# Performance work log

Hardware: AMD Instinct MI355X
Metric: run time of the kernel (lower is better)

Reference implementation:

```python
import jax, jax.numpy as jnp
import numpy as np

END_CLAUSE, PRED, ARG_FUNC, ARG_VAR = 0, 1, 2, 3
NUM_ACTION_TYPES = 8
NUM_LAYERS = 3


def _ln(x, g, b, eps=1e-5):
    m = jnp.mean(x, -1, keepdims=True)
    v = jnp.var(x, -1, keepdims=True)
    return (x - m) * jax.lax.rsqrt(v + eps) * g + b


def _ssm_block(x, Win, b_in, Wdt, b_dt, Alog, WB, b_B, WC, b_C, Dp, Wout, b_out, g, b):
    # x: [B,T,D]
    res = x
    xz = x @ Win.T + b_in
    x_ssm, z = jnp.split(xz, 2, axis=-1)
    z = jax.nn.silu(z)
    dt = jax.nn.softplus(x_ssm @ Wdt.T + b_dt)   # [B,T,D]
    Bm = x_ssm @ WB.T + b_B                       # [B,T,N]
    Cm = x_ssm @ WC.T + b_C                       # [B,T,N]
    A = -jnp.exp(Alog)                            # [D,N]

    def step(h, inp):
        x_t, dt_t, B_t, C_t = inp                 # [B,D],[B,D],[B,N],[B,N]
        dA = jnp.exp(A[None] * dt_t[:, :, None])  # [B,D,N]
        h = dA * h + (dt_t * x_t)[:, :, None] * B_t[:, None, :]
        return h, jnp.einsum('bdn,bn->bd', h, C_t)

    h0 = jnp.zeros((x.shape[0], Alog.shape[0], Alog.shape[1]), x.dtype)
    xs = tuple(jnp.swapaxes(a, 0, 1) for a in (x_ssm, dt, Bm, Cm))
    _, ys = jax.lax.scan(step, h0, xs)
    y = jnp.swapaxes(ys, 0, 1)                    # [B,T,D]
    y = (y + Dp * x_ssm) * z
    y = y @ Wout.T + b_out
    return _ln(y + res, g, b)


def _forward(symbol_embeds, memory, action_embed, W_arg, b_arg, var_embed, W_comb, b_comb,
             Win, b_in, Wdt, b_dt, Alog, WB, b_B, WC, b_C, Dp, Wout, b_out, ssm_g, ssm_b,
             Wm, b_m, Wg, b_g, cn_g, cn_b, Wa, b_a, Wq, b_q, Wk, b_k, Wv, b_v,
             target_actions, target_arguments, symbol_mask):
    B, T = target_actions.shape
    S = symbol_embeds.shape[1]
    D = symbol_embeds.shape[2]
    MV = var_embed.shape[0]
    # teacher-forcing shift with END_CLAUSE BOS
    dec_a = jnp.concatenate([jnp.full((B, 1), END_CLAUSE, target_actions.dtype), target_actions[:, :-1]], 1)
    dec_g = jnp.concatenate([jnp.zeros((B, 1), target_arguments.dtype), target_arguments[:, :-1]], 1)
    act_emb = action_embed[dec_a]                                          # [B,T,D]
    sym = symbol_embeds[jnp.arange(B)[:, None], jnp.clip(dec_g, 0, S - 1)]  # [B,T,D]
    ptr_emb = sym @ W_arg.T + b_arg
    var_emb_t = var_embed[jnp.clip(dec_g, 0, MV - 1)]
    ptr_mask = (dec_a == PRED) | (dec_a == ARG_FUNC)
    vmask = dec_a == ARG_VAR
    arg_emb = jnp.where(ptr_mask[..., None], ptr_emb,
                        jnp.where(vmask[..., None], var_emb_t, jnp.zeros((), symbol_embeds.dtype)))
    h = jnp.concatenate([act_emb, arg_emb], -1) @ W_comb.T + b_comb
    mem_summary = memory.mean(1)  # zero padding included, matching torch code
    for l in range(NUM_LAYERS):
        h = _ssm_block(h, Win[l], b_in[l], Wdt[l], b_dt[l], Alog[l], WB[l], b_B[l], WC[l], b_C[l],
                       Dp[l], Wout[l], b_out[l], ssm_g[l], ssm_b[l])
        ctx = jnp.broadcast_to((mem_summary @ Wm[l].T + b_m[l])[:, None, :], h.shape)
        gate = jax.nn.sigmoid(jnp.concatenate([h, ctx], -1) @ Wg[l].T + b_g[l])
        h = _ln(h + gate * ctx, cn_g[l], cn_b[l])
    action_logits = h @ Wa.T + b_a
    scores = jnp.einsum('btd,bsd->bts', h @ Wq.T + b_q, symbol_embeds @ Wk.T + b_k) / (float(D) ** 0.5)
    scores = jnp.where(symbol_mask[:, None, :], scores, -jnp.inf)
    var_logits = h @ Wv.T + b_v
    return action_logits, scores, var_logits


def setup_inputs() -> dict:
    B, T, S, M, D, N, L, NA, MV = 8, 1024, 128, 512, 512, 16, NUM_LAYERS, NUM_ACTION_TYPES, 20
    keys = iter(jax.random.split(jax.random.key(0), 48))

    def nrm(shape, scale=1.0):
        return jax.random.normal(next(keys), shape, jnp.float32) * scale

    s = 1.0 / np.sqrt(D)
    s2 = 1.0 / np.sqrt(2 * D)
    inp = dict(
        symbol_embeds=nrm((B, S, D)), memory=nrm((B, M, D)),
        action_embed=nrm((NA, D), 0.02), W_arg=nrm((D, D), s), b_arg=jnp.zeros((D,)),
        var_embed=nrm((MV, D), 0.02), W_comb=nrm((D, 2 * D), s2), b_comb=jnp.zeros((D,)),
        Win=nrm((L, 2 * D, D), s), b_in=jnp.zeros((L, 2 * D)),
        Wdt=nrm((L, D, D), s), b_dt=jnp.zeros((L, D)),
        Alog=nrm((L, D, N)),
        WB=nrm((L, N, D), s), b_B=jnp.zeros((L, N)),
        WC=nrm((L, N, D), s), b_C=jnp.zeros((L, N)),
        Dp=jnp.ones((L, D)),
        Wout=nrm((L, D, D), s), b_out=jnp.zeros((L, D)),
        ssm_g=jnp.ones((L, D)), ssm_b=jnp.zeros((L, D)),
        Wm=nrm((L, D, D), s), b_m=jnp.zeros((L, D)),
        Wg=nrm((L, D, 2 * D), s2), b_g=jnp.zeros((L, D)),
        cn_g=jnp.ones((L, D)), cn_b=jnp.zeros((L, D)),
        Wa=nrm((NA, D), s), b_a=jnp.zeros((NA,)),
        Wq=nrm((D, D), s), b_q=jnp.zeros((D,)),
        Wk=nrm((D, D), s), b_k=jnp.zeros((D,)),
        Wv=nrm((MV, D), s), b_v=jnp.zeros((MV,)),
        target_actions=jax.random.randint(next(keys), (B, T), 0, NA),
        target_arguments=jax.random.randint(next(keys), (B, T), 0, S),
    )
    counts = jax.random.randint(next(keys), (B,), S // 2, S + 1)
    inp['symbol_mask'] = jnp.arange(S)[None, :] < counts[:, None]
    return inp


def reference(symbol_embeds, memory, action_embed, W_arg, b_arg, var_embed, W_comb, b_comb,
              Win, b_in, Wdt, b_dt, Alog, WB, b_B, WC, b_C, Dp, Wout, b_out, ssm_g, ssm_b,
              Wm, b_m, Wg, b_g, cn_g, cn_b, Wa, b_a, Wq, b_q, Wk, b_k, Wv, b_v,
              target_actions, target_arguments, symbol_mask):
    return _forward(symbol_embeds, memory, action_embed, W_arg, b_arg, var_embed, W_comb, b_comb,
                    Win, b_in, Wdt, b_dt, Alog, WB, b_B, WC, b_C, Dp, Wout, b_out, ssm_g, ssm_b,
                    Wm, b_m, Wg, b_g, cn_g, cn_b, Wa, b_a, Wq, b_q, Wk, b_k, Wv, b_v,
                    target_actions, target_arguments, symbol_mask)
```

## Files before the change

### kernel.cpp

```cpp
#include <hip/hip_runtime.h>
#include <math.h>

#define R_  8192
#define T_  1024
#define B_  8
#define S_  128
#define D_  512
#define N_  16
#define MV_ 20
#define NA_ 8
#define MM_ 512

#define TC  4
#define LCH 256
#define TS  32
#define DB  8

typedef __attribute__((ext_vector_type(8))) short short8;
typedef __attribute__((ext_vector_type(4))) float f32x4;

static __device__ __forceinline__ float sigmoidf_(float x) {
  return 1.f / (1.f + __expf(-x));
}

static __device__ __forceinline__ void split2(float x0, float x1,
                                              unsigned& hp, unsigned& lp) {
  unsigned u0 = __float_as_uint(x0), u1 = __float_as_uint(x1);
  unsigned r0 = u0 + 0x7fffu + ((u0 >> 16) & 1u);
  unsigned r1 = u1 + 0x7fffu + ((u1 >> 16) & 1u);
  hp = __builtin_amdgcn_perm(r1, r0, 0x07060302u);
  float l0 = x0 - __uint_as_float(r0 & 0xffff0000u);
  float l1 = x1 - __uint_as_float(r1 & 0xffff0000u);
  lp = __builtin_amdgcn_perm(__float_as_uint(l1), __float_as_uint(l0),
                             0x07060302u);
}

static __device__ __forceinline__ float row16_sum(float v) {
  v += __int_as_float(__builtin_amdgcn_update_dpp(0, __float_as_int(v), 0xB1, 0xF, 0xF, true));
  v += __int_as_float(__builtin_amdgcn_update_dpp(0, __float_as_int(v), 0x4E, 0xF, 0xF, true));
  v += __int_as_float(__builtin_amdgcn_update_dpp(0, __float_as_int(v), 0x141, 0xF, 0xF, true));
  v += __int_as_float(__builtin_amdgcn_update_dpp(0, __float_as_int(v), 0x140, 0xF, 0xF, true));
  return v;
}

#define KP 40

__global__ void __launch_bounds__(256) gemm_bx3(
    const float* __restrict__ A, int lda,
    const unsigned short* __restrict__ Wh, const unsigned short* __restrict__ Wl,
    const float* __restrict__ bias,
    const float* __restrict__ bbias,
    float* __restrict__ C, int ldc,
    int K, int act,
    float* __restrict__ aux1, float* __restrict__ aux2)
{
  __shared__ unsigned short Ah[128 * KP], Al[128 * KP];
  __shared__ unsigned short Bh[64 * KP],  Bl[64 * KP];
  const int tid = threadIdx.x;
  const int m0 = blockIdx.y << 7;
  const int n0 = blockIdx.x << 6;
  const int lane = tid & 63;
  const int wm = ((tid >> 6) & 1) << 6;
  const int wn = (tid >> 7) << 5;
  const int lr = lane & 15, quad = lane >> 4;

  const int arow = tid >> 1, akoff = (tid & 1) << 4;
  const float* ap = A + (size_t)(m0 + arow) * lda + akoff;
  const int brow = tid >> 2, bkoff = (tid & 3) << 3;
  const unsigned short* wph = Wh + (size_t)(n0 + brow) * K + bkoff;
  const unsigned short* wpl = Wl + (size_t)(n0 + brow) * K + bkoff;

  f32x4 acc[4][2];
#pragma unroll
  for (int mt = 0; mt < 4; ++mt)
#pragma unroll
    for (int nt = 0; nt < 2; ++nt)
      acc[mt][nt] = (f32x4){0.f, 0.f, 0.f, 0.f};

  for (int k0 = 0; k0 < K; k0 += 32) {
    float4 av[4];
#pragma unroll
    for (int i = 0; i < 4; ++i) av[i] = *(const float4*)(ap + k0 + (i << 2));
    uint4 bh = *(const uint4*)(wph + k0);
    uint4 bl = *(const uint4*)(wpl + k0);
    __syncthreads();
    {
      float af[16] = {av[0].x, av[0].y, av[0].z, av[0].w,
                      av[1].x, av[1].y, av[1].z, av[1].w,
                      av[2].x, av[2].y, av[2].z, av[2].w,
                      av[3].x, av[3].y, av[3].z, av[3].w};
#pragma unroll
      for (int g = 0; g < 2; ++g) {
        unsigned h4[4], l4[4];
#pragma unroll
        for (int p = 0; p < 4; ++p)
          split2(af[g * 8 + 2 * p], af[g * 8 + 2 * p + 1], h4[p], l4[p]);
        *(uint4*)&Ah[arow * KP + akoff + (g << 3)] = make_uint4(h4[0], h4[1], h4[2], h4[3]);
        *(uint4*)&Al[arow * KP + akoff + (g << 3)] = make_uint4(l4[0], l4[1], l4[2], l4[3]);
      }
    }
    *(uint4*)&Bh[brow * KP + bkoff] = bh;
    *(uint4*)&Bl[brow * KP + bkoff] = bl;
    __syncthreads();

    short8 fah[4], fal[4], fbh[2], fbl[2];
#pragma unroll
    for (int mt = 0; mt < 4; ++mt) {
      int r = (wm + mt * 16 + lr) * KP + quad * 8;
      fah[mt] = *(const short8*)&Ah[r];
      fal[mt] = *(const short8*)&Al[r];
    }
#pragma unroll
    for (int nt = 0; nt < 2; ++nt) {
      int r = (wn + nt * 16 + lr) * KP + quad * 8;
      fbh[nt] = *(const short8*)&Bh[r];
      fbl[nt] = *(const short8*)&Bl[r];
    }
#pragma unroll
    for (int mt = 0; mt < 4; ++mt)
#pragma unroll
      for (int nt = 0; nt < 2; ++nt) {
        acc[mt][nt] = __builtin_amdgcn_mfma_f32_16x16x32_bf16(
            fah[mt], fbl[nt], acc[mt][nt], 0, 0, 0);
        acc[mt][nt] = __builtin_amdgcn_mfma_f32_16x16x32_bf16(
            fal[mt], fbh[nt], acc[mt][nt], 0, 0, 0);
        acc[mt][nt] = __builtin_amdgcn_mfma_f32_16x16x32_bf16(
            fah[mt], fbh[nt], acc[mt][nt], 0, 0, 0);
      }
  }

  const int bb = m0 >> 10;
#pragma unroll
  for (int mt = 0; mt < 4; ++mt)
#pragma unroll
    for (int nt = 0; nt < 2; ++nt) {
      int ncol = n0 + wn + nt * 16 + lr;
      float bv = bias ? bias[ncol] : 0.f;
      if (bbias) bv += bbias[(size_t)bb * ldc + ncol];
#pragma unroll
      for (int reg = 0; reg < 4; ++reg) {
        int m = m0 + wm + mt * 16 + quad * 4 + reg;
        float v = acc[mt][nt][reg] + bv;
        if (act == 0) {
          C[(size_t)m * ldc + ncol] = v;
        } else if (act == 1) {
          C[(size_t)m * ldc + ncol] = (v > 20.f) ? v : log1pf(__expf(v));
        } else if (act == 2) {
          C[(size_t)m * ldc + ncol] = sigmoidf_(v);
        } else if (act == 3) {
          if (ncol < 512)      C[(size_t)m * 512 + ncol] = (v > 20.f) ? v : log1pf(__expf(v));
          else if (ncol < 528) aux1[(size_t)m * 16 + (ncol - 512)] = v;
          else if (ncol < 544) aux2[(size_t)m * 16 + (ncol - 528)] = v;
        } else {
          if (ncol < 512)      C[(size_t)m * 512 + ncol] = v;
          else if (ncol < 520) aux1[(size_t)m * 8 + (ncol - 512)] = v;
          else if (ncol < 540) aux2[(size_t)m * 20 + (ncol - 520)] = v;
        }
      }
    }
}

__global__ void wcvt(const float* __restrict__ W, int ldw,
                     unsigned short* __restrict__ hi, unsigned short* __restrict__ lo)
{
  int gid = blockIdx.x * 256 + threadIdx.x;
  int base = gid << 3;
  int r = base >> 9, c = base & 511;
  const float* p = W + (size_t)r * ldw + c;
  float4 a0 = *(const float4*)p, a1 = *(const float4*)(p + 4);
  float af[8] = {a0.x, a0.y, a0.z, a0.w, a1.x, a1.y, a1.z, a1.w};
  unsigned h4[4], l4[4];
#pragma unroll
  for (int p2 = 0; p2 < 4; ++p2) split2(af[2 * p2], af[2 * p2 + 1], h4[p2], l4[p2]);
  *(uint4*)&hi[(size_t)r * 512 + c] = make_uint4(h4[0], h4[1], h4[2], h4[3]);
  *(uint4*)&lo[(size_t)r * 512 + c] = make_uint4(l4[0], l4[1], l4[2], l4[3]);
}

__global__ void pack_w_bf(unsigned short* __restrict__ hi, unsigned short* __restrict__ lo,
                          float* __restrict__ bd,
                          const float* __restrict__ w0, const float* __restrict__ b0,
                          const float* __restrict__ w1, const float* __restrict__ b1,
                          const float* __restrict__ w2, const float* __restrict__ b2,
                          int n1, int n2)
{
  int gid = blockIdx.x * 256 + threadIdx.x;
  int base = gid << 3;
  int r = base >> 9, c = base & 511;
  const float* src = nullptr;
  if (r < 512)                 src = w0 + (size_t)r * 512 + c;
  else if (r < 512 + n1)       src = w1 + (size_t)(r - 512) * 512 + c;
  else if (r < 512 + n1 + n2)  src = w2 + (size_t)(r - 512 - n1) * 512 + c;
  float af[8] = {0.f};
  if (src) {
    float4 a0 = *(const float4*)src, a1 = *(const float4*)(src + 4);
    af[0]=a0.x; af[1]=a0.y; af[2]=a0.z; af[3]=a0.w;
    af[4]=a1.x; af[5]=a1.y; af[6]=a1.z; af[7]=a1.w;
  }
  unsigned h4[4], l4[4];
#pragma unroll
  for (int p2 = 0; p2 < 4; ++p2) split2(af[2 * p2], af[2 * p2 + 1], h4[p2], l4[p2]);
  *(uint4*)&hi[(size_t)r * 512 + c] = make_uint4(h4[0], h4[1], h4[2], h4[3]);
  *(uint4*)&lo[(size_t)r * 512 + c] = make_uint4(l4[0], l4[1], l4[2], l4[3]);
  if (c == 0) {
    float bvv = 0.f;
    if (r < 512)                 bvv = b0[r];
    else if (r < 512 + n1)       bvv = b1[r - 512];
    else if (r < 512 + n1 + n2)  bvv = b2[r - 512 - n1];
    bd[r] = bvv;
  }
}

#define BM 64
#define BN 64
#define BK 16

__global__ void __launch_bounds__(256) scores_kernel(
    const float* __restrict__ q, const float* __restrict__ kmat,
    const int* __restrict__ mask, float* __restrict__ out)
{
  __shared__ __align__(16) float As[BK][BM + 4];
  __shared__ __align__(16) float Ws[BK][BN + 4];
  const int b = blockIdx.z;
  const float* A = q + (size_t)b * T_ * D_;
  const float* W = kmat + (size_t)b * S_ * D_;
  const int tid = threadIdx.x;
  const int m0 = blockIdx.y * BM;
  const int n0 = blockIdx.x * BN;
  const int tx = tid & 15, ty = tid >> 4;
  const int lr = tid >> 2;
  const int lk = (tid & 3) << 2;
  float acc[4][4] = {{0.f}};
  const float* aptr = A + (size_t)(m0 + lr) * D_ + lk;
  const float* wptr = W + (size_t)(n0 + lr) * D_ + lk;

  for (int k0 = 0; k0 < D_; k0 += BK) {
    float4 av = *(const float4*)(aptr + k0);
    float4 wv = *(const float4*)(wptr + k0);
    __syncthreads();
    As[lk + 0][lr] = av.x; As[lk + 1][lr] = av.y;
    As[lk + 2][lr] = av.z; As[lk + 3][lr] = av.w;
    Ws[lk + 0][lr] = wv.x; Ws[lk + 1][lr] = wv.y;
    Ws[lk + 2][lr] = wv.z; Ws[lk + 3][lr] = wv.w;
    __syncthreads();
#pragma unroll
    for (int kk = 0; kk < BK; ++kk) {
      float4 a4 = *(const float4*)&As[kk][ty << 2];
      float4 b4 = *(const float4*)&Ws[kk][tx << 2];
      float a_[4] = {a4.x, a4.y, a4.z, a4.w};
      float b_[4] = {b4.x, b4.y, b4.z, b4.w};
#pragma unroll
      for (int i = 0; i < 4; ++i)
#pragma unroll
        for (int j = 0; j < 4; ++j)
          acc[i][j] = fmaf(a_[i], b_[j], acc[i][j]);
    }
  }

  const float scale = 0.044194173824159216f;
#pragma unroll
  for (int i = 0; i < 4; ++i) {
    int t = m0 + (ty << 2) + i;
#pragma unroll
    for (int j = 0; j < 4; ++j) {
      int s = n0 + (tx << 2) + j;
      float v = acc[i][j] * scale;
      if (mask[b * S_ + s] == 0) v = -1e30f;
      out[((size_t)(b * T_ + t)) * S_ + s] = v;
    }
  }
}

__global__ void gemm_small(const float* __restrict__ A, int lda,
                           const float* __restrict__ W, int ldw,
                           const float* __restrict__ bias,
                           float* __restrict__ C, int ldc,
                           int MN, int Ncols, int K)
{
  int gid = blockIdx.x * 256 + threadIdx.x;
  if (gid >= MN) return;
  int r = gid / Ncols, o = gid - r * Ncols;
  const float4* a = (const float4*)(A + (size_t)r * lda);
  const float4* w = (const float4*)(W + (size_t)o * ldw);
  float acc = bias ? bias[o] : 0.f;
  int K4 = K >> 2;
  for (int k = 0; k < K4; ++k) {
    float4 av = a[k], wv = w[k];
    acc = fmaf(av.x, wv.x, fmaf(av.y, wv.y, fmaf(av.z, wv.z, fmaf(av.w, wv.w, acc))));
  }
  C[(size_t)r * ldc + o] = acc;
}

__global__ void ctx_kernel(const float* __restrict__ msum, const float* __restrict__ Wm,
                           const float* __restrict__ b_m, float* __restrict__ ctxv)
{
  int gid = blockIdx.x * 256 + threadIdx.x;
  int l = gid >> 12, b = (gid >> 9) & 7, dd = gid & 511;
  const float4* a = (const float4*)(msum + b * 512);
  const float4* w = (const float4*)(Wm + ((size_t)l * 512 + dd) * 512);
  float acc = b_m[l * 512 + dd];
  for (int k = 0; k < 128; ++k) {
    float4 av = a[k], wv = w[k];
    acc = fmaf(av.x, wv.x, fmaf(av.y, wv.y, fmaf(av.z, wv.z, fmaf(av.w, wv.w, acc))));
  }
  ctxv[gid] = acc;
}

__global__ void gctx_kernel(const float* __restrict__ ctxv, const float* __restrict__ Wg,
                            const float* __restrict__ b_g, float* __restrict__ gctx)
{
  int gid = blockIdx.x * 256 + threadIdx.x;
  int l = gid >> 12, b = (gid >> 9) & 7, dd = gid & 511;
  const float4* a = (const float4*)(ctxv + ((size_t)l * 8 + b) * 512);
  const float4* w = (const float4*)(Wg + ((size_t)l * 512 + dd) * 1024 + 512);
  float acc = b_g[l * 512 + dd];
  for (int k = 0; k < 128; ++k) {
    float4 av = a[k], wv = w[k];
    acc = fmaf(av.x, wv.x, fmaf(av.y, wv.y, fmaf(av.z, wv.z, fmaf(av.w, wv.w, acc))));
  }
  gctx[gid] = acc;
}

__global__ void __launch_bounds__(256) transpose512(
    const float* __restrict__ A, float* __restrict__ At)
{
  __shared__ float tl[32][33];
  int i0 = blockIdx.y * 32, j0 = blockIdx.x * 32;
  int li = threadIdx.x & 31, lj = threadIdx.x >> 5;
#pragma unroll
  for (int k = 0; k < 4; ++k)
    tl[lj * 4 + k][li] = A[(size_t)(i0 + lj * 4 + k) * 512 + j0 + li];
  __syncthreads();
#pragma unroll
  for (int k = 0; k < 4; ++k)
    At[(size_t)(j0 + lj * 4 + k) * 512 + i0 + li] = tl[li][lj * 4 + k];
}

__global__ void memsum_kernel(const float* __restrict__ mem, float* __restrict__ out)
{
  int b = blockIdx.x >> 1;
  int d = ((blockIdx.x & 1) << 8) + threadIdx.x;
  const float* p = mem + (size_t)b * MM_ * D_ + d;
  float s = 0.f;
  for (int m = 0; m < MM_; ++m) s += p[(size_t)m * D_];
  out[b * D_ + d] = s * (1.f / MM_);
}

__global__ void combine_kernel(float* __restrict__ h, const float* __restrict__ Psym,
                               const float* __restrict__ Pact,
                               const float* __restrict__ Pvar, const float* __restrict__ b2,
                               const float* __restrict__ bcomb,
                               const int* __restrict__ ta, const int* __restrict__ tg)
{
  int i = blockIdx.x * 256 + threadIdx.x;
  int r = i >> 9, j = i & 511;
  int t = r & (T_ - 1);
  int a = t ? ta[r - 1] : 0;
  float val = Pact[a * D_ + j] + bcomb[j];
  if (a == 1 || a == 2) {
    int g = t ? tg[r - 1] : 0;
    g = g < 0 ? 0 : (g > S_ - 1 ? S_ - 1 : g);
    val += Psym[((size_t)(r >> 10) * S_ + g) * D_ + j] + b2[j];
  } else if (a == 3) {
    int g = t ? tg[r - 1] : 0;
    g = g < 0 ? 0 : (g > MV_ - 1 ? MV_ - 1 : g);
    val += Pvar[g * D_ + j];
  }
  h[i] = val;
}

__global__ void __launch_bounds__(128) scan_pass1(
    const float* __restrict__ xz, const float* __restrict__ dts,
    const float* __restrict__ Bmv, const float* __restrict__ Alog,
    float* __restrict__ aprod, float* __restrict__ hend)
{
  __shared__ __align__(8) float sdt[TS][DB];
  __shared__ __align__(8) float sx[TS][DB];
  __shared__ __align__(16) float sB[TS][16];
  const int tid = threadIdx.x;
  const int n = tid & 15, dl = tid >> 4;
  const int c = blockIdx.x, db = blockIdx.y, b = blockIdx.z;
  const int d = (db << 3) + dl;
  const int t0 = c * LCH;
  const int lrow = tid >> 2;
  const int lc2 = (tid & 3) << 1;
  const int bc4 = (tid & 3) << 2;

  float An = -__expf(Alog[d * N_ + n]);
  float hst = 0.f, dsum = 0.f;

  for (int tt = 0; tt < LCH; tt += TS) {
    __syncthreads();
    {
      size_t gr = (size_t)b * T_ + t0 + tt + lrow;
      *(float2*)&sdt[lrow][lc2] = *(const float2*)&dts[(gr << 9) + (db << 3) + lc2];
      *(float2*)&sx[lrow][lc2]  = *(const float2*)&xz[(gr << 10) + (db << 3) + lc2];
      *(float4*)&sB[lrow][bc4]  = *(const float4*)&Bmv[gr * N_ + bc4];
    }
    __syncthreads();
#pragma unroll 8
    for (int s = 0; s < TS; ++s) {
      float dtv = sdt[s][dl], xv = sx[s][dl], Bv = sB[s][n];
      float dA = __expf(An * dtv);
      hst = fmaf(dA, hst, dtv * xv * Bv);
      dsum += dtv;
    }
  }
  size_t idx = (size_t)c * (B_ * D_ * N_) + ((size_t)b * D_ + d) * N_ + n;
  aprod[idx] = __expf(An * dsum);
  hend[idx]  = hst;
}

__global__ void scan_pass2(const float* __restrict__ aprod, float* __restrict__ hs)
{
  int g = blockIdx.x * 256 + threadIdx.x;
  float prev = 0.f;
  for (int c = 0; c < TC; ++c) {
    size_t idx = (size_t)c * (B_ * D_ * N_) + g;
    float a = aprod[idx], he = hs[idx];
    hs[idx] = prev;
    prev = fmaf(a, prev, he);
  }
}

__global__ void __launch_bounds__(128) scan_pass3(
    const float* __restrict__ xz, float* __restrict__ dy,
    const float* __restrict__ Bmv, const float* __restrict__ Cmv,
    const float* __restrict__ Alog, const float* __restrict__ hstart,
    const float* __restrict__ Dp)
{
  __shared__ __align__(8) float sdt[TS][DB];
  __shared__ __align__(8) float sx[TS][DB];
  __shared__ __align__(8) float sz[TS][DB];
  __shared__ __align__(16) float sB[TS][16];
  __shared__ __align__(16) float sC[TS][16];
  const int tid = threadIdx.x;
  const int n = tid & 15, dl = tid >> 4;
  const int c = blockIdx.x, db = blockIdx.y, b = blockIdx.z;
  const int d = (db << 3) + dl;
  const int t0 = c * LCH;
  const int lrow = tid >> 2;
  const int lc2 = (tid & 3) << 1;
  const int bc4 = (tid & 3) << 2;

  float An = -__expf(Alog[d * N_ + n]);
  float Dpd = Dp[d];
  size_t sidx = (size_t)c * (B_ * D_ * N_) + ((size_t)b * D_ + d) * N_ + n;
  float hst = hstart[sidx];

  for (int tt = 0; tt < LCH; tt += TS) {
    __syncthreads();
    {
      size_t gr = (size_t)b * T_ + t0 + tt + lrow;
      *(float2*)&sdt[lrow][lc2] = *(const float2*)&dy[(gr << 9) + (db << 3) + lc2];
      *(float2*)&sx[lrow][lc2]  = *(const float2*)&xz[(gr << 10) + (db << 3) + lc2];
      *(float2*)&sz[lrow][lc2]  = *(const float2*)&xz[(gr << 10) + D_ + (db << 3) + lc2];
      *(float4*)&sB[lrow][bc4]  = *(const float4*)&Bmv[gr * N_ + bc4];
      *(float4*)&sC[lrow][bc4]  = *(const float4*)&Cmv[gr * N_ + bc4];
    }
    __syncthreads();
#pragma unroll 8
    for (int s = 0; s < TS; ++s) {
      float dtv = sdt[s][dl], xv = sx[s][dl];
      float Bv = sB[s][n], Cv = sC[s][n];
      float dA = __expf(An * dtv);
      hst = fmaf(dA, hst, dtv * xv * Bv);
      float cc = row16_sum(hst * Cv);
      if (n == 0) {
        float zv = sz[s][dl];
        sdt[s][dl] = (cc + Dpd * xv) * (zv * sigmoidf_(zv));
      }
    }
    __syncthreads();
    {
      size_t gr = (size_t)b * T_ + t0 + tt + lrow;
      *(float2*)&dy[(gr << 9) + (db << 3) + lc2] = *(const float2*)&sdt[lrow][lc2];
    }
  }
}

__global__ void __launch_bounds__(256) ln_kernel(
    float* __restrict__ h, const float* __restrict__ add,
    const float* __restrict__ ctx,
    const float* __restrict__ gw, const float* __restrict__ bw, int mode)
{
  int r = (blockIdx.x << 2) + (threadIdx.x >> 6);
  int lane = threadIdx.x & 63;
  int b = r >> 10;
  size_t base = (size_t)r * D_;
  float v[8];
#pragma unroll
  for (int k = 0; k < 8; ++k) {
    int j = lane + (k << 6);
    float x = h[base + j];
    float a = add[base + j];
    v[k] = mode ? fmaf(a, ctx[b * D_ + j], x) : (x + a);
  }
  float s = 0.f;
#pragma unroll
  for (int k = 0; k < 8; ++k) s += v[k];
#pragma unroll
  for (int o = 1; o < 64; o <<= 1) s += __shfl_xor(s, o, 64);
  float mean = s * (1.f / D_);
  float vs = 0.f;
#pragma unroll
  for (int k = 0; k < 8; ++k) { float d = v[k] - mean; vs = fmaf(d, d, vs); }
#pragma unroll
  for (int o = 1; o < 64; o <<= 1) vs += __shfl_xor(vs, o, 64);
  float inv = 1.0f / sqrtf(vs * (1.f / D_) + 1e-5f);
#pragma unroll
  for (int k = 0; k < 8; ++k) {
    int j = lane + (k << 6);
    h[base + j] = (v[k] - mean) * inv * gw[j] + bw[j];
  }
}

extern "C" void kernel_launch(void* const* d_in, const int* in_sizes, int n_in,
                              void* d_out, int out_size, void* d_ws, size_t ws_size,
                              hipStream_t stream)
{
  const float* symbol_embeds = (const float*)d_in[0];
  const float* memory_       = (const float*)d_in[1];
  const float* action_embed  = (const float*)d_in[2];
  const float* W_arg  = (const float*)d_in[3];
  const float* b_arg  = (const float*)d_in[4];
  const float* var_embed = (const float*)d_in[5];
  const float* W_comb = (const float*)d_in[6];
  const float* b_comb = (const float*)d_in[7];
  const float* Win  = (const float*)d_in[8];
  const float* b_in = (const float*)d_in[9];
  const float* Wdt  = (const float*)d_in[10];
  const float* b_dt = (const float*)d_in[11];
  const float* Alog = (const float*)d_in[12];
  const float* WB   = (const float*)d_in[13];
  const float* b_B  = (const float*)d_in[14];
  const float* WC   = (const float*)d_in[15];
  const float* b_C  = (const float*)d_in[16];
  const float* Dp   = (const float*)d_in[17];
  const float* Wout = (const float*)d_in[18];
  const float* b_out= (const float*)d_in[19];
  const float* ssm_g= (const float*)d_in[20];
  const float* ssm_b= (const float*)d_in[21];
  const float* Wm   = (const float*)d_in[22];
  const float* b_m  = (const float*)d_in[23];
  const float* Wg   = (const float*)d_in[24];
  const float* b_g  = (const float*)d_in[25];
  const float* cn_g = (const float*)d_in[26];
  const float* cn_b = (const float*)d_in[27];
  const float* Wa   = (const float*)d_in[28];
  const float* b_a  = (const float*)d_in[29];
  const float* Wq   = (const float*)d_in[30];
  const float* b_q  = (const float*)d_in[31];
  const float* Wk   = (const float*)d_in[32];
  const float* b_k  = (const float*)d_in[33];
  const float* Wv   = (const float*)d_in[34];
  const float* b_v  = (const float*)d_in[35];
  const int* ta     = (const int*)d_in[36];
  const int* tg     = (const int*)d_in[37];
  const int* smask  = (const int*)d_in[38];
  (void)in_sizes; (void)n_in; (void)out_size; (void)ws_size;

  float* ws = (float*)d_ws;
  float* xz = ws;
  float* dy = xz + (size_t)R_ * 1024;
  float* h  = dy + (size_t)R_ * 512;
  float* Psym = xz;

  float* out     = (float*)d_out;
  float* out_act = out;
  float* out_sc  = out + (size_t)R_ * NA_;
  float* out_var = out + (size_t)R_ * (NA_ + S_);

  float* Bmv  = out;
  float* Cmv  = Bmv  + 131072;
  float* aprd = Cmv  + 131072;
  float* hend = aprd + 262144;
  float* Wpk  = hend + 262144;
  float* bpk  = Wpk  + 294912;
  float* msum = bpk  + 576;
  float* ctxv = msum + 4096;
  float* gctx = ctxv + 12288;

  unsigned short* WpkH = (unsigned short*)Wpk;
  unsigned short* WpkL = WpkH + 294912;
  unsigned short* WinH = (unsigned short*)aprd;
  unsigned short* WinL = WinH + 524288;
  unsigned short* WsqH = (unsigned short*)aprd;
  unsigned short* WsqL = WsqH + 262144;
  unsigned short* WgH  = (unsigned short*)hend;
  unsigned short* WgL  = WgH + 262144;
  unsigned short* PrepH = (unsigned short*)Bmv;
  unsigned short* PrepL = PrepH + 262144;

  float* Pact = aprd;
  float* Pvar = Pact + 4096;
  float* b2   = Pvar + 10240;
  float* M2   = hend;
  float* WargT= Wpk;

  dim3 blk(256), blk128(128);

  memsum_kernel<<<16, blk, 0, stream>>>(memory_, msum);
  gemm_small<<<16, blk, 0, stream>>>(action_embed, 512, W_comb, 1024, nullptr,
                                     Pact, 512, 8 * 512, 512, 512);
  gemm_small<<<40, blk, 0, stream>>>(var_embed, 512, W_comb + 512, 1024, nullptr,
                                     Pvar, 512, 20 * 512, 512, 512);
  gemm_small<<<2, blk, 0, stream>>>(b_arg, 512, W_comb + 512, 1024, nullptr,
                                    b2, 512, 512, 512, 512);
  ctx_kernel<<<48, blk, 0, stream>>>(msum, Wm, b_m, ctxv);
  gctx_kernel<<<48, blk, 0, stream>>>(ctxv, Wg, b_g, gctx);
  transpose512<<<dim3(16, 16), blk, 0, stream>>>(W_arg, WargT);
  wcvt<<<128, blk, 0, stream>>>(WargT, 512, PrepH, PrepL);
  gemm_bx3<<<dim3(8, 4), blk, 0, stream>>>(W_comb + 512, 1024, PrepH, PrepL,
                                           nullptr, nullptr, M2, 512, 512, 0,
                                           nullptr, nullptr);
  wcvt<<<128, blk, 0, stream>>>(M2, 512, PrepH, PrepL);
  gemm_bx3<<<dim3(8, 8), blk, 0, stream>>>(symbol_embeds, 512, PrepH, PrepL,
                                           nullptr, nullptr, Psym, 512, 512, 0,
                                           nullptr, nullptr);
  combine_kernel<<<R_ * 512 / 256, blk, 0, stream>>>(h, Psym, Pact, Pvar, b2,
                                                     b_comb, ta, tg);

  for (int l = 0; l < 3; ++l) {
    const float* Win_l  = Win  + (size_t)l * 1024 * 512;
    const float* b_in_l = b_in + l * 1024;
    const float* Wdt_l  = Wdt  + (size_t)l * 512 * 512;
    const float* b_dt_l = b_dt + l * 512;
    const float* Alog_l = Alog + (size_t)l * 512 * 16;
    const float* WB_l   = WB   + (size_t)l * 16 * 512;
    const float* b_B_l  = b_B  + l * 16;
    const float* WC_l   = WC   + (size_t)l * 16 * 512;
    const float* b_C_l  = b_C  + l * 16;
    const float* Dp_l   = Dp   + l * 512;
    const float* Wout_l = Wout + (size_t)l * 512 * 512;
    const float* b_out_l= b_out+ l * 512;
    const float* ssm_g_l= ssm_g+ l * 512;
    const float* ssm_b_l= ssm_b+ l * 512;
    const float* Wg_l   = Wg   + (size_t)l * 512 * 1024;
    const float* cn_g_l = cn_g + l * 512;
    const float* cn_b_l = cn_b + l * 512;

    wcvt<<<256, blk, 0, stream>>>(Win_l, 512, WinH, WinL);
    pack_w_bf<<<144, blk, 0, stream>>>(WpkH, WpkL, bpk, Wdt_l, b_dt_l,
                                       WB_l, b_B_l, WC_l, b_C_l, 16, 16);
    gemm_bx3<<<dim3(16, 64), blk, 0, stream>>>(h, 512, WinH, WinL,
                                               b_in_l, nullptr, xz, 1024, 512, 0,
                                               nullptr, nullptr);
    gemm_bx3<<<dim3(9, 64), blk, 0, stream>>>(xz, 1024, WpkH, WpkL,
                                              bpk, nullptr, dy, 512, 512, 3,
                                              Bmv, Cmv);
    scan_pass1<<<dim3(TC, D_ / DB, B_), blk128, 0, stream>>>(xz, dy, Bmv, Alog_l,
                                                             aprd, hend);
    scan_pass2<<<B_ * D_ * N_ / 256, blk, 0, stream>>>(aprd, hend);
    scan_pass3<<<dim3(TC, D_ / DB, B_), blk128, 0, stream>>>(xz, dy, Bmv, Cmv,
                                                             Alog_l, hend, Dp_l);
    wcvt<<<128, blk, 0, stream>>>(Wout_l, 512, WsqH, WsqL);
    gemm_bx3<<<dim3(8, 64), blk, 0, stream>>>(dy, 512, WsqH, WsqL,
                                              b_out_l, nullptr, xz, 512, 512, 0,
                                              nullptr, nullptr);
    ln_kernel<<<2048, blk, 0, stream>>>(h, xz, nullptr, ssm_g_l, ssm_b_l, 0);
    wcvt<<<128, blk, 0, stream>>>(Wg_l, 1024, WgH, WgL);
    gemm_bx3<<<dim3(8, 64), blk, 0, stream>>>(h, 512, WgH, WgL,
                                              nullptr, gctx + l * 4096, dy, 512, 512, 2,
                                              nullptr, nullptr);
    ln_kernel<<<2048, blk, 0, stream>>>(h, dy, ctxv + l * 4096, cn_g_l, cn_b_l, 1);
  }

  pack_w_bf<<<144, blk, 0, stream>>>(WpkH, WpkL, bpk, Wq, b_q, Wa, b_a,
                                     Wv, b_v, NA_, MV_);
  gemm_bx3<<<dim3(9, 64), blk, 0, stream>>>(h, 512, WpkH, WpkL,
                                            bpk, nullptr, xz, 512, 512, 4,
                                            out_act, out_var);
  wcvt<<<128, blk, 0, stream>>>(Wk, 512, WsqH, WsqL);
  gemm_bx3<<<dim3(8, 8), blk, 0, stream>>>(symbol_embeds, 512, WsqH, WsqL,
                                           b_k, nullptr, dy, 512, 512, 0,
                                           nullptr, nullptr);
  scores_kernel<<<dim3(2, 16, 8), blk, 0, stream>>>(xz, dy, smask, out_sc);
}
```

Baseline: 1.276 ms.

## Merge weight-conversion launches and restructure scan passes with transposed LDS staging

Combines several separate weight bf16 hi/lo conversion kernels into single launches per stage, cutting launch count. The two selective-scan kernels now stage dt/x/z transposed in shared memory and load each thread's 32 timesteps into registers with vector loads. In pass 3 the per-step DPP row reduction and predicated write are replaced by writing h*C terms to a padded shared buffer and reducing 16 terms per thread in batches of 16 steps. This adds more barriers and shared memory usage, and may increase register pressure from the fully unrolled register arrays.

```diff
diff --git a/kernel.cpp b/kernel.cpp
--- a/kernel.cpp
+++ b/kernel.cpp
@@ -15,6 +15,7 @@
 #define LCH 256
 #define TS  32
 #define DB  8
+#define TP  36
 
 typedef __attribute__((ext_vector_type(8))) short short8;
 typedef __attribute__((ext_vector_type(4))) float f32x4;
@@ -33,14 +34,6 @@
   float l1 = x1 - __uint_as_float(r1 & 0xffff0000u);
   lp = __builtin_amdgcn_perm(__float_as_uint(l1), __float_as_uint(l0),
                              0x07060302u);
-}
-
-static __device__ __forceinline__ float row16_sum(float v) {
-  v += __int_as_float(__builtin_amdgcn_update_dpp(0, __float_as_int(v), 0xB1, 0xF, 0xF, true));
-  v += __int_as_float(__builtin_amdgcn_update_dpp(0, __float_as_int(v), 0x4E, 0xF, 0xF, true));
-  v += __int_as_float(__builtin_amdgcn_update_dpp(0, __float_as_int(v), 0x141, 0xF, 0xF, true));
-  v += __int_as_float(__builtin_amdgcn_update_dpp(0, __float_as_int(v), 0x140, 0xF, 0xF, true));
-  return v;
 }
 
 #define KP 40
@@ -160,10 +153,10 @@
     }
 }
 
-__global__ void wcvt(const float* __restrict__ W, int ldw,
-                     unsigned short* __restrict__ hi, unsigned short* __restrict__ lo)
-{
-  int gid = blockIdx.x * 256 + threadIdx.x;
+static __device__ __forceinline__ void wcvt_body(
+    int gid, const float* __restrict__ W, int ldw,
+    unsigned short* __restrict__ hi, unsigned short* __restrict__ lo)
+{
   int base = gid << 3;
   int r = base >> 9, c = base & 511;
   const float* p = W + (size_t)r * ldw + c;
@@ -176,14 +169,14 @@
   *(uint4*)&lo[(size_t)r * 512 + c] = make_uint4(l4[0], l4[1], l4[2], l4[3]);
 }
 
-__global__ void pack_w_bf(unsigned short* __restrict__ hi, unsigned short* __restrict__ lo,
-                          float* __restrict__ bd,
-                          const float* __restrict__ w0, const float* __restrict__ b0,
-                          const float* __restrict__ w1, const float* __restrict__ b1,
-                          const float* __restrict__ w2, const float* __restrict__ b2,
-                          int n1, int n2)
-{
-  int gid = blockIdx.x * 256 + threadIdx.x;
+static __device__ __forceinline__ void pack_body(
+    int gid, unsigned short* __restrict__ hi, unsigned short* __restrict__ lo,
+    float* __restrict__ bd,
+    const float* __restrict__ w0, const float* __restrict__ b0,
+    const float* __restrict__ w1, const float* __restrict__ b1,
+    const float* __restrict__ w2, const float* __restrict__ b2,
+    int n1, int n2)
+{
   int base = gid << 3;
   int r = base >> 9, c = base & 511;
   const float* src = nullptr;
@@ -208,6 +201,54 @@
     else if (r < 512 + n1 + n2)  bvv = b2[r - 512 - n1];
     bd[r] = bvv;
   }
+}
+
+__global__ void cvt_layerA(const float* __restrict__ Win_l,
+                           const float* __restrict__ Wdt_l, const float* __restrict__ b_dt_l,
+                           const float* __restrict__ WB_l, const float* __restrict__ b_B_l,
+                           const float* __restrict__ WC_l, const float* __restrict__ b_C_l,
+                           unsigned short* WinH, unsigned short* WinL,
+                           unsigned short* WpkH, unsigned short* WpkL, float* bpk)
+{
+  int blk = blockIdx.x;
+  if (blk < 256)
+    wcvt_body(blk * 256 + threadIdx.x, Win_l, 512, WinH, WinL);
+  else
+    pack_body((blk - 256) * 256 + threadIdx.x, WpkH, WpkL, bpk,
+              Wdt_l, b_dt_l, WB_l, b_B_l, WC_l, b_C_l, 16, 16);
+}
+
+__global__ void cvt_layerB(const float* __restrict__ Wout_l,
+                           const float* __restrict__ Wg_l,
+                           unsigned short* WsqH, unsigned short* WsqL,
+                           unsigned short* WgH, unsigned short* WgL)
+{
+  int blk = blockIdx.x;
+  if (blk < 128)
+    wcvt_body(blk * 256 + threadIdx.x, Wout_l, 512, WsqH, WsqL);
+  else
+    wcvt_body((blk - 128) * 256 + threadIdx.x, Wg_l, 1024, WgH, WgL);
+}
+
+__global__ void cvt_heads(const float* __restrict__ Wq, const float* __restrict__ b_q,
+                          const float* __restrict__ Wa, const float* __restrict__ b_a,
+                          const float* __restrict__ Wv, const float* __restrict__ b_v,
+                          const float* __restrict__ Wk,
+                          unsigned short* WpkH, unsigned short* WpkL, float* bpk,
+                          unsigned short* WsqH, unsigned short* WsqL)
+{
+  int blk = blockIdx.x;
+  if (blk < 144)
+    pack_body(blk * 256 + threadIdx.x, WpkH, WpkL, bpk,
+              Wq, b_q, Wa, b_a, Wv, b_v, NA_, MV_);
+  else
+    wcvt_body((blk - 144) * 256 + threadIdx.x, Wk, 512, WsqH, WsqL);
+}
+
+__global__ void wcvt(const float* __restrict__ W, int ldw,
+                     unsigned short* __restrict__ hi, unsigned short* __restrict__ lo)
+{
+  wcvt_body(blockIdx.x * 256 + threadIdx.x, W, ldw, hi, lo);
 }
 
 #define BM 64
@@ -373,17 +414,15 @@
     const float* __restrict__ Bmv, const float* __restrict__ Alog,
     float* __restrict__ aprod, float* __restrict__ hend)
 {
-  __shared__ __align__(8) float sdt[TS][DB];
-  __shared__ __align__(8) float sx[TS][DB];
+  __shared__ __align__(16) float sdtT[DB][TP];
+  __shared__ __align__(16) float sxT[DB][TP];
   __shared__ __align__(16) float sB[TS][16];
   const int tid = threadIdx.x;
   const int n = tid & 15, dl = tid >> 4;
   const int c = blockIdx.x, db = blockIdx.y, b = blockIdx.z;
   const int d = (db << 3) + dl;
   const int t0 = c * LCH;
-  const int lrow = tid >> 2;
-  const int lc2 = (tid & 3) << 1;
-  const int bc4 = (tid & 3) << 2;
+  const int lrow = tid >> 2, lc2 = (tid & 3) << 1, bc4 = (tid & 3) << 2;
 
   float An = -__expf(Alog[d * N_ + n]);
   float hst = 0.f, dsum = 0.f;
@@ -392,17 +431,25 @@
     __syncthreads();
     {
       size_t gr = (size_t)b * T_ + t0 + tt + lrow;
-      *(float2*)&sdt[lrow][lc2] = *(const float2*)&dts[(gr << 9) + (db << 3) + lc2];
-      *(float2*)&sx[lrow][lc2]  = *(const float2*)&xz[(gr << 10) + (db << 3) + lc2];
-      *(float4*)&sB[lrow][bc4]  = *(const float4*)&Bmv[gr * N_ + bc4];
+      float2 dt2 = *(const float2*)&dts[(gr << 9) + (db << 3) + lc2];
+      float2 x2  = *(const float2*)&xz[(gr << 10) + (db << 3) + lc2];
+      sdtT[lc2][lrow] = dt2.x; sdtT[lc2 + 1][lrow] = dt2.y;
+      sxT[lc2][lrow]  = x2.x;  sxT[lc2 + 1][lrow]  = x2.y;
+      *(float4*)&sB[lrow][bc4] = *(const float4*)&Bmv[gr * N_ + bc4];
     }
     __syncthreads();
-#pragma unroll 8
+    float dtr[TS], xr[TS];
+#pragma unroll
+    for (int qv = 0; qv < TS / 4; ++qv) {
+      *(float4*)&dtr[qv << 2] = *(const float4*)&sdtT[dl][qv << 2];
+      *(float4*)&xr[qv << 2]  = *(const float4*)&sxT[dl][qv << 2];
+    }
+#pragma unroll
     for (int s = 0; s < TS; ++s) {
-      float dtv = sdt[s][dl], xv = sx[s][dl], Bv = sB[s][n];
-      float dA = __expf(An * dtv);
-      hst = fmaf(dA, hst, dtv * xv * Bv);
-      dsum += dtv;
+      float Bv = sB[s][n];
+      float dA = __expf(An * dtr[s]);
+      hst = fmaf(dA, hst, dtr[s] * xr[s] * Bv);
+      dsum += dtr[s];
     }
   }
   size_t idx = (size_t)c * (B_ * D_ * N_) + ((size_t)b * D_ + d) * N_ + n;
@@ -422,28 +469,30 @@
   }
 }
 
+#define HPAD 20
+
 __global__ void __launch_bounds__(128) scan_pass3(
     const float* __restrict__ xz, float* __restrict__ dy,
     const float* __restrict__ Bmv, const float* __restrict__ Cmv,
     const float* __restrict__ Alog, const float* __restrict__ hstart,
     const float* __restrict__ Dp)
 {
-  __shared__ __align__(8) float sdt[TS][DB];
-  __shared__ __align__(8) float sx[TS][DB];
-  __shared__ __align__(8) float sz[TS][DB];
+  __shared__ __align__(16) float sdtT[DB][TP];
+  __shared__ __align__(16) float sxT[DB][TP];
+  __shared__ __align__(16) float szT[DB][TP];
   __shared__ __align__(16) float sB[TS][16];
   __shared__ __align__(16) float sC[TS][16];
+  __shared__ __align__(16) float sterm[128][HPAD];
   const int tid = threadIdx.x;
   const int n = tid & 15, dl = tid >> 4;
   const int c = blockIdx.x, db = blockIdx.y, b = blockIdx.z;
   const int d = (db << 3) + dl;
   const int t0 = c * LCH;
-  const int lrow = tid >> 2;
-  const int lc2 = (tid & 3) << 1;
-  const int bc4 = (tid & 3) << 2;
+  const int lrow = tid >> 2, lc2 = (tid & 3) << 1, bc4 = (tid & 3) << 2;
+  const int rsi = tid >> 3, rdl = tid & 7;
 
   float An = -__expf(Alog[d * N_ + n]);
-  float Dpd = Dp[d];
+  float Dpr = Dp[(db << 3) + rdl];
   size_t sidx = (size_t)c * (B_ * D_ * N_) + ((size_t)b * D_ + d) * N_ + n;
   float hst = hstart[sidx];
 
@@ -451,29 +500,57 @@
     __syncthreads();
     {
       size_t gr = (size_t)b * T_ + t0 + tt + lrow;
-      *(float2*)&sdt[lrow][lc2] = *(const float2*)&dy[(gr << 9) + (db << 3) + lc2];
-      *(float2*)&sx[lrow][lc2]  = *(const float2*)&xz[(gr << 10) + (db << 3) + lc2];
-      *(float2*)&sz[lrow][lc2]  = *(const float2*)&xz[(gr << 10) + D_ + (db << 3) + lc2];
-      *(float4*)&sB[lrow][bc4]  = *(const float4*)&Bmv[gr * N_ + bc4];
-      *(float4*)&sC[lrow][bc4]  = *(const float4*)&Cmv[gr * N_ + bc4];
+      float2 dt2 = *(const float2*)&dy[(gr << 9) + (db << 3) + lc2];
+      float2 x2  = *(const float2*)&xz[(gr << 10) + (db << 3) + lc2];
+      float2 z2  = *(const float2*)&xz[(gr << 10) + D_ + (db << 3) + lc2];
+      sdtT[lc2][lrow] = dt2.x; sdtT[lc2 + 1][lrow] = dt2.y;
+      sxT[lc2][lrow]  = x2.x;  sxT[lc2 + 1][lrow]  = x2.y;
+      szT[lc2][lrow]  = z2.x;  szT[lc2 + 1][lrow]  = z2.y;
+      *(float4*)&sB[lrow][bc4] = *(const float4*)&Bmv[gr * N_ + bc4];
+      *(float4*)&sC[lrow][bc4] = *(const float4*)&Cmv[gr * N_ + bc4];
     }
     __syncthreads();
-#pragma unroll 8
-    for (int s = 0; s < TS; ++s) {
-      float dtv = sdt[s][dl], xv = sx[s][dl];
-      float Bv = sB[s][n], Cv = sC[s][n];
-      float dA = __expf(An * dtv);
-      hst = fmaf(dA, hst, dtv * xv * Bv);
-      float cc = row16_sum(hst * Cv);
-      if (n == 0) {
-        float zv = sz[s][dl];
-        sdt[s][dl] = (cc + Dpd * xv) * (zv * sigmoidf_(zv));
+    float dtr[TS], xr[TS];
+#pragma unroll
+    for (int qv = 0; qv < TS / 4; ++qv) {
+      *(float4*)&dtr[qv << 2] = *(const float4*)&sdtT[dl][qv << 2];
+      *(float4*)&xr[qv << 2]  = *(const float4*)&sxT[dl][qv << 2];
+    }
+#pragma unroll
+    for (int half = 0; half < 2; ++half) {
+      const int hs = half << 4;
+#pragma unroll
+      for (int si = 0; si < 16; ++si) {
+        int s = hs + si;
+        float Bv = sB[s][n], Cv = sC[s][n];
+        float dA = __expf(An * dtr[s]);
+        hst = fmaf(dA, hst, dtr[s] * xr[s] * Bv);
+        sterm[(si << 3) + dl][n] = hst * Cv;
       }
-    }
-    __syncthreads();
+      __syncthreads();
+      {
+        float4 t0v = *(const float4*)&sterm[tid][0];
+        float4 t1v = *(const float4*)&sterm[tid][4];
+        float4 t2v = *(const float4*)&sterm[tid][8];
+        float4 t3v = *(const float4*)&sterm[tid][12];
+        float s16 = ((t0v.x + t0v.y) + (t0v.z + t0v.w))
+                  + ((t1v.x + t1v.y) + (t1v.z + t1v.w))
+                  + ((t2v.x + t2v.y) + (t2v.z + t2v.w))
+                  + ((t3v.x + t3v.y) + (t3v.z + t3v.w));
+        float zv = szT[rdl][hs + rsi];
+        float xv = sxT[rdl][hs + rsi];
+        float yv = (s16 + Dpr * xv) * (zv * sigmoidf_(zv));
+        __syncthreads();
+        sdtT[rdl][hs + rsi] = yv;
+      }
+      __syncthreads();
+    }
     {
       size_t gr = (size_t)b * T_ + t0 + tt + lrow;
-      *(float2*)&dy[(gr << 9) + (db << 3) + lc2] = *(const float2*)&sdt[lrow][lc2];
+      float2 y2;
+      y2.x = sdtT[lc2][lrow];
+      y2.y = sdtT[lc2 + 1][lrow];
+      *(float2*)&dy[(gr << 9) + (db << 3) + lc2] = y2;
     }
   }
 }
@@ -503,7 +580,7 @@
   float mean = s * (1.f / D_);
   float vs = 0.f;
 #pragma unroll
-  for (int k = 0; k < 8; ++k) { float d = v[k] - mean; vs = fmaf(d, d, vs); }
+  for (int k = 0; k < 8; ++k) { float dv = v[k] - mean; vs = fmaf(dv, dv, vs); }
 #pragma unroll
   for (int o = 1; o < 64; o <<= 1) vs += __shfl_xor(vs, o, 64);
   float inv = 1.0f / sqrtf(vs * (1.f / D_) + 1e-5f);
@@ -639,9 +716,8 @@
     const float* cn_g_l = cn_g + l * 512;
     const float* cn_b_l = cn_b + l * 512;
 
-    wcvt<<<256, blk, 0, stream>>>(Win_l, 512, WinH, WinL);
-    pack_w_bf<<<144, blk, 0, stream>>>(WpkH, WpkL, bpk, Wdt_l, b_dt_l,
-                                       WB_l, b_B_l, WC_l, b_C_l, 16, 16);
+    cvt_layerA<<<400, blk, 0, stream>>>(Win_l, Wdt_l, b_dt_l, WB_l, b_B_l,
+                                        WC_l, b_C_l, WinH, WinL, WpkH, WpkL, bpk);
     gemm_bx3<<<dim3(16, 64), blk, 0, stream>>>(h, 512, WinH, WinL,
                                                b_in_l, nullptr, xz, 1024, 512, 0,
                                                nullptr, nullptr);
@@ -653,24 +729,22 @@
     scan_pass2<<<B_ * D_ * N_ / 256, blk, 0, stream>>>(aprd, hend);
     scan_pass3<<<dim3(TC, D_ / DB, B_), blk128, 0, stream>>>(xz, dy, Bmv, Cmv,
                                                              Alog_l, hend, Dp_l);
-    wcvt<<<128, blk, 0, stream>>>(Wout_l, 512, WsqH, WsqL);
+    cvt_layerB<<<256, blk, 0, stream>>>(Wout_l, Wg_l, WsqH, WsqL, WgH, WgL);
     gemm_bx3<<<dim3(8, 64), blk, 0, stream>>>(dy, 512, WsqH, WsqL,
                                               b_out_l, nullptr, xz, 512, 512, 0,
                                               nullptr, nullptr);
     ln_kernel<<<2048, blk, 0, stream>>>(h, xz, nullptr, ssm_g_l, ssm_b_l, 0);
-    wcvt<<<128, blk, 0, stream>>>(Wg_l, 1024, WgH, WgL);
     gemm_bx3<<<dim3(8, 64), blk, 0, stream>>>(h, 512, WgH, WgL,
                                               nullptr, gctx + l * 4096, dy, 512, 512, 2,
                                               nullptr, nullptr);
     ln_kernel<<<2048, blk, 0, stream>>>(h, dy, ctxv + l * 4096, cn_g_l, cn_b_l, 1);
   }
 
-  pack_w_bf<<<144, blk, 0, stream>>>(WpkH, WpkL, bpk, Wq, b_q, Wa, b_a,
-                                     Wv, b_v, NA_, MV_);
+  cvt_heads<<<272, blk, 0, stream>>>(Wq, b_q, Wa, b_a, Wv, b_v, Wk,
+                                     WpkH, WpkL, bpk, WsqH, WsqL);
   gemm_bx3<<<dim3(9, 64), blk, 0, stream>>>(h, 512, WpkH, WpkL,
                                             bpk, nullptr, xz, 512, 512, 4,
                                             out_act, out_var);
-  wcvt<<<128, blk, 0, stream>>>(Wk, 512, WsqH, WsqL);
   gemm_bx3<<<dim3(8, 8), blk, 0, stream>>>(symbol_embeds, 512, WsqH, WsqL,
                                            b_k, nullptr, dy, 512, 512, 0,
                                            nullptr, nullptr);
```

Measured after the change: 1.171 ms. -8.3%, faster.
